# Performance work log

Hardware: AMD Instinct MI355X
Metric: run time of the kernel (lower is better)

The kernel has to match this reference:

```python
import jax, jax.numpy as jnp
import numpy as np
from jax import lax

DN = ('NCHW', 'OIHW', 'NCHW')


def setup_inputs() -> dict:
    key = jax.random.key(0)
    k1, k2 = jax.random.split(key)
    x = jax.random.uniform(k1, (32, 3, 128, 128), dtype=jnp.float32)
    # kaiming-uniform-like filters; the module zeroes the first filter after init
    fan_in = 1 * 7 * 7
    bound = np.sqrt(6.0 / ((1 + 5.0) * fan_in))  # kaiming_uniform with a=sqrt(5)
    weight = jax.random.uniform(k2, (512, 1, 7, 7), minval=-bound, maxval=bound,
                                dtype=jnp.float32)
    weight = weight.at[0].set(0.0)
    std = jnp.asarray(2.0, dtype=jnp.float32)
    return {"x": x, "weight": weight, "std": std}


def _rbf_dist_conv(gray, weight, std, stride=1):
    # ||window - filter||^2 = ||window||^2 + ||filter||^2 - 2 * window . filter
    strides = (stride, stride)
    xw = lax.conv_general_dilated(gray, weight, strides, 'VALID',
                                  dimension_numbers=DN)       # [B,O,OH,OW]
    ones_k = jnp.ones((1, 1) + weight.shape[2:], gray.dtype)
    x2 = lax.conv_general_dilated(gray * gray, ones_k, strides, 'VALID',
                                  dimension_numbers=DN)       # [B,1,OH,OW]
    w2 = jnp.sum(weight * weight, axis=(1, 2, 3))[None, :, None, None]
    sq = jnp.maximum(x2 + w2 - 2.0 * xw, 0.0)
    dist = jnp.sqrt(sq)                                        # torch.cdist
    # gauss RBF: exp(-d^2 / (2*std^2))
    return jnp.exp(-(dist * dist) / (2.0 * std * std))


def reference(x, weight, std):
    # forward converts 3-channel input to grayscale (ITU-R 601 weights, as torchvision)
    gray = (0.2989 * x[:, 0] + 0.587 * x[:, 1] + 0.114 * x[:, 2])[:, None]  # [B,1,H,W]
    return _rbf_dist_conv(gray, weight, std, stride=1)
```

## Files before the change

### kernel.cpp

```cpp
#include <hip/hip_runtime.h>

typedef _Float16 half_t;
typedef __attribute__((ext_vector_type(8))) _Float16 half8;
typedef __attribute__((ext_vector_type(4))) float f32x4;

#define NB 32
#define NH 128
#define NW 128
#define NOH 122
#define NOW 122
#define NOC 512
#define NTAP 49
#define KPAD 64


__global__ __launch_bounds__(256) void k_gray(const float* __restrict__ x,
                                              half_t* __restrict__ gh) {
    int t = blockIdx.x * 256 + threadIdx.x;
    if (t >= NB * NH * NW) return;
    int b = t >> 14;
    int pix = t & 16383;
    const float* xb = x + (size_t)b * 3 * 16384;
    float g = 0.2989f * xb[pix] + 0.587f * xb[16384 + pix] + 0.114f * xb[32768 + pix];
    gh[t] = (half_t)g;
}

__global__ __launch_bounds__(64) void k_w(const float* __restrict__ w,
                                          half_t* __restrict__ Wh,
                                          float* __restrict__ w2) {
    int o = blockIdx.x * 64 + threadIdx.x;
    if (o >= NOC) return;
    float s = 0.f;
    for (int t = 0; t < KPAD; ++t) {
        float v = (t < NTAP) ? w[o * NTAP + t] : 0.f;
        half_t h = (half_t)v;
        Wh[o * KPAD + t] = h;
        float f = (float)h;
        s += f * f;
    }
    w2[o] = s;
}

__global__ __launch_bounds__(256) void k_x2(const half_t* __restrict__ gh,
                                            float* __restrict__ x2) {
    int t = blockIdx.x * 256 + threadIdx.x;
    if (t >= NB * NOH * NOW) return;
    int b = t / (NOH * NOW);
    int rem = t - b * (NOH * NOW);
    int oh = rem / NOW;
    int ow = rem - oh * NOW;
    const half_t* g = gh + ((size_t)b * NH + oh) * NW + ow;
    float s = 0.f;
#pragma unroll
    for (int kh = 0; kh < 7; ++kh) {
#pragma unroll
        for (int kw = 0; kw < 7; ++kw) {
            float v = (float)g[kh * NW + kw];
            s += v * v;
        }
    }
    x2[t] = s;
}

__global__ __launch_bounds__(256) void k_main(const half_t* __restrict__ gh,
                                              const half_t* __restrict__ Wh,
                                              const float* __restrict__ w2,
                                              const float* __restrict__ x2,
                                              const float* __restrict__ stdp,
                                              float* __restrict__ out) {
    const int fg = blockIdx.x;
    const int oh = blockIdx.y;
    const int b  = blockIdx.z;

    __shared__ half_t gS[10][136];

    const int tid = threadIdx.x;
    for (int idx = tid; idx < 10 * 136; idx += 256) {
        int r = idx / 136;
        int c = idx - r * 136;
        half_t hv = (half_t)0.f;
        if (r < 7 && c < 128) hv = gh[((size_t)b * NH + (oh + r)) * NW + c];
        gS[r][c] = hv;
    }

    const int wave = tid >> 6;
    const int lane = tid & 63;
    const int col  = lane & 15;
    const int kq   = lane >> 4;
    const int n0   = wave * 32;

    half8 afrag[4][2];
#pragma unroll
    for (int mi = 0; mi < 4; ++mi) {
#pragma unroll
        for (int ks = 0; ks < 2; ++ks) {
            const half_t* ap = Wh + ((size_t)(fg * 64 + mi * 16 + col) * KPAD + ks * 32 + kq * 8);
            afrag[mi][ks] = *(const half8*)ap;
        }
    }

    __syncthreads();

    half8 bfrag[2][2];
#pragma unroll
    for (int ni = 0; ni < 2; ++ni) {
#pragma unroll
        for (int ks = 0; ks < 2; ++ks) {
            half8 v;
#pragma unroll
            for (int i = 0; i < 8; ++i) {
                int t = ks * 32 + kq * 8 + i;
                int kh = (t * 37) >> 8;
                int kw = t - kh * 7;
                v[i] = gS[kh][n0 + ni * 16 + col + kw];
            }
            bfrag[ni][ks] = v;
        }
    }

    f32x4 acc[4][2];
#pragma unroll
    for (int mi = 0; mi < 4; ++mi)
#pragma unroll
        for (int ni = 0; ni < 2; ++ni) {
            f32x4 z = {0.f, 0.f, 0.f, 0.f};
            acc[mi][ni] = z;
        }

#pragma unroll
    for (int ks = 0; ks < 2; ++ks)
#pragma unroll
        for (int mi = 0; mi < 4; ++mi)
#pragma unroll
            for (int ni = 0; ni < 2; ++ni)
                acc[mi][ni] = __builtin_amdgcn_mfma_f32_16x16x32_f16(
                    afrag[mi][ks], bfrag[ni][ks], acc[mi][ni], 0, 0, 0);

    const float sv = stdp[0];
    const float inv2s2 = 0.5f / (sv * sv);

#pragma unroll
    for (int ni = 0; ni < 2; ++ni) {
        const int p = n0 + ni * 16 + col;
        const bool pok = p < NOW;
        const float x2v = pok ? x2[((size_t)b * NOH + oh) * NOW + p] : 0.f;
#pragma unroll
        for (int mi = 0; mi < 4; ++mi) {
#pragma unroll
            for (int r = 0; r < 4; ++r) {
                const int o = fg * 64 + mi * 16 + kq * 4 + r;
                float sq = x2v + w2[o] - 2.f * acc[mi][ni][r];
                sq = fmaxf(sq, 0.f);
                float res = __expf(-sq * inv2s2);
                if (pok) out[(((size_t)b * NOC + o) * NOH + oh) * NOW + p] = res;
            }
        }
    }
}

extern "C" void kernel_launch(void* const* d_in, const int* in_sizes, int n_in,
                              void* d_out, int out_size, void* d_ws, size_t ws_size,
                              hipStream_t stream) {
    const float* x    = (const float*)d_in[0];
    const float* w    = (const float*)d_in[1];
    const float* stdp = (const float*)d_in[2];
    float* out = (float*)d_out;

    char* ws = (char*)d_ws;
    half_t* gh = (half_t*)ws;
    half_t* Wh = (half_t*)(ws + 1048576);
    float*  w2 = (float*)(ws + 1114112);
    float*  x2 = (float*)(ws + 1116160);

    k_gray<<<(NB * NH * NW + 255) / 256, 256, 0, stream>>>(x, gh);
    k_w<<<(NOC + 63) / 64, 64, 0, stream>>>(w, Wh, w2);
    k_x2<<<(NB * NOH * NOW + 255) / 256, 256, 0, stream>>>(gh, x2);

    dim3 grid(8, NOH, NB);
    k_main<<<grid, 256, 0, stream>>>(gh, Wh, w2, x2, stdp, out);
}
```

Measured before the change: 367.4 us.

## Process multiple output rows per block with rolling LDS row buffer

Each block now handles a chunk of 31 output rows instead of one. It keeps an 8-row ring buffer of the grayscale image in shared memory and loads only one new row per iteration. Filter fragments and per-filter squared norms are loaded once into registers and reused across all rows, removing redundant global and LDS fill work per row. The trade-off is a grid shrunk from about 31k blocks to 1024, which lowers parallelism and the number of stores in flight for what is largely an output-write-bound kernel. It also adds a barrier per row.

New measurement: 408.5 us. 1.11x slower.

```diff
diff --git a/kernel.cpp b/kernel.cpp
--- a/kernel.cpp
+++ b/kernel.cpp
@@ -12,6 +12,8 @@
 #define NOC 512
 #define NTAP 49
 #define KPAD 64
+#define NCH 4
+#define RPC 31
 
 
 __global__ __launch_bounds__(256) void k_gray(const float* __restrict__ x,
@@ -69,20 +71,14 @@
                                               const float* __restrict__ stdp,
                                               float* __restrict__ out) {
     const int fg = blockIdx.x;
-    const int oh = blockIdx.y;
+    const int ch = blockIdx.y;
     const int b  = blockIdx.z;
+    const int oh0 = ch * RPC;
+    const int nrows = (NOH - oh0 < RPC) ? (NOH - oh0) : RPC;
 
-    __shared__ half_t gS[10][136];
+    __shared__ half_t gS[8][136];
 
-    const int tid = threadIdx.x;
-    for (int idx = tid; idx < 10 * 136; idx += 256) {
-        int r = idx / 136;
-        int c = idx - r * 136;
-        half_t hv = (half_t)0.f;
-        if (r < 7 && c < 128) hv = gh[((size_t)b * NH + (oh + r)) * NW + c];
-        gS[r][c] = hv;
-    }
-
+    const int tid  = threadIdx.x;
     const int wave = tid >> 6;
     const int lane = tid & 63;
     const int col  = lane & 15;
@@ -91,68 +87,88 @@
 
     half8 afrag[4][2];
 #pragma unroll
-    for (int mi = 0; mi < 4; ++mi) {
+    for (int mi = 0; mi < 4; ++mi)
 #pragma unroll
         for (int ks = 0; ks < 2; ++ks) {
             const half_t* ap = Wh + ((size_t)(fg * 64 + mi * 16 + col) * KPAD + ks * 32 + kq * 8);
             afrag[mi][ks] = *(const half8*)ap;
         }
-    }
 
-    __syncthreads();
+    f32x4 w2c[4];
+#pragma unroll
+    for (int mi = 0; mi < 4; ++mi)
+        w2c[mi] = *(const f32x4*)(w2 + fg * 64 + mi * 16 + kq * 4);
 
-    half8 bfrag[2][2];
-#pragma unroll
-    for (int ni = 0; ni < 2; ++ni) {
-#pragma unroll
-        for (int ks = 0; ks < 2; ++ks) {
-            half8 v;
-#pragma unroll
-            for (int i = 0; i < 8; ++i) {
-                int t = ks * 32 + kq * 8 + i;
-                int kh = (t * 37) >> 8;
-                int kw = t - kh * 7;
-                v[i] = gS[kh][n0 + ni * 16 + col + kw];
-            }
-            bfrag[ni][ks] = v;
+    for (int idx = tid; idx < 7 * 136; idx += 256) {
+        int r = idx / 136;
+        int c = idx - r * 136;
+        if (r < 6) {
+            half_t hv = (c < 128) ? gh[((size_t)b * NH + (oh0 + r)) * NW + c] : (half_t)0.f;
+            gS[(oh0 + r) & 7][c] = hv;
+        } else {
+            gS[(oh0 + 7) & 7][c] = (half_t)0.f;
         }
     }
-
-    f32x4 acc[4][2];
-#pragma unroll
-    for (int mi = 0; mi < 4; ++mi)
-#pragma unroll
-        for (int ni = 0; ni < 2; ++ni) {
-            f32x4 z = {0.f, 0.f, 0.f, 0.f};
-            acc[mi][ni] = z;
-        }
-
-#pragma unroll
-    for (int ks = 0; ks < 2; ++ks)
-#pragma unroll
-        for (int mi = 0; mi < 4; ++mi)
-#pragma unroll
-            for (int ni = 0; ni < 2; ++ni)
-                acc[mi][ni] = __builtin_amdgcn_mfma_f32_16x16x32_f16(
-                    afrag[mi][ks], bfrag[ni][ks], acc[mi][ni], 0, 0, 0);
 
     const float sv = stdp[0];
     const float inv2s2 = 0.5f / (sv * sv);
 
+    for (int oh = oh0; oh < oh0 + nrows; ++oh) {
+        if (tid < 136) {
+            int row = oh + 6;
+            half_t hv = (tid < 128) ? gh[((size_t)b * NH + row) * NW + tid] : (half_t)0.f;
+            gS[row & 7][tid] = hv;
+        }
+        __syncthreads();
+
+        half8 bfrag[2][2];
 #pragma unroll
-    for (int ni = 0; ni < 2; ++ni) {
-        const int p = n0 + ni * 16 + col;
-        const bool pok = p < NOW;
-        const float x2v = pok ? x2[((size_t)b * NOH + oh) * NOW + p] : 0.f;
+        for (int ni = 0; ni < 2; ++ni)
 #pragma unroll
-        for (int mi = 0; mi < 4; ++mi) {
+            for (int ks = 0; ks < 2; ++ks) {
+                half8 v;
 #pragma unroll
-            for (int r = 0; r < 4; ++r) {
-                const int o = fg * 64 + mi * 16 + kq * 4 + r;
-                float sq = x2v + w2[o] - 2.f * acc[mi][ni][r];
-                sq = fmaxf(sq, 0.f);
-                float res = __expf(-sq * inv2s2);
-                if (pok) out[(((size_t)b * NOC + o) * NOH + oh) * NOW + p] = res;
+                for (int i = 0; i < 8; ++i) {
+                    int t = ks * 32 + kq * 8 + i;
+                    int kh = (t * 37) >> 8;
+                    int kw = t - kh * 7;
+                    v[i] = gS[(oh + kh) & 7][n0 + ni * 16 + col + kw];
+                }
+                bfrag[ni][ks] = v;
+            }
+
+        f32x4 acc[4][2];
+#pragma unroll
+        for (int mi = 0; mi < 4; ++mi)
+#pragma unroll
+            for (int ni = 0; ni < 2; ++ni) {
+                f32x4 z = {0.f, 0.f, 0.f, 0.f};
+                acc[mi][ni] = z;
+            }
+
+#pragma unroll
+        for (int ks = 0; ks < 2; ++ks)
+#pragma unroll
+            for (int mi = 0; mi < 4; ++mi)
+#pragma unroll
+                for (int ni = 0; ni < 2; ++ni)
+                    acc[mi][ni] = __builtin_amdgcn_mfma_f32_16x16x32_f16(
+                        afrag[mi][ks], bfrag[ni][ks], acc[mi][ni], 0, 0, 0);
+
+#pragma unroll
+        for (int ni = 0; ni < 2; ++ni) {
+            const int p = n0 + ni * 16 + col;
+            const bool pok = p < NOW;
+            const float x2v = pok ? x2[((size_t)b * NOH + oh) * NOW + p] : 0.f;
+#pragma unroll
+            for (int mi = 0; mi < 4; ++mi) {
+#pragma unroll
+                for (int r = 0; r < 4; ++r) {
+                    const int o = fg * 64 + mi * 16 + kq * 4 + r;
+                    float sq = fmaxf(fmaf(-2.f, acc[mi][ni][r], x2v + w2c[mi][r]), 0.f);
+                    float res = __expf(-sq * inv2s2);
+                    if (pok) out[(((size_t)b * NOC + o) * NOH + oh) * NOW + p] = res;
+                }
             }
         }
     }
@@ -176,6 +192,6 @@
     k_w<<<(NOC + 63) / 64, 64, 0, stream>>>(w, Wh, w2);
     k_x2<<<(NB * NOH * NOW + 255) / 256, 256, 0, stream>>>(gh, x2);
 
-    dim3 grid(8, NOH, NB);
+    dim3 grid(8, NCH, NB);
     k_main<<<grid, 256, 0, stream>>>(gh, Wh, w2, x2, stdp, out);
 }
```

## Pad filter taps to 8x8 and swap MFMA operands for vectorized output stores

Applied to the files above, without the earlier changes.

Filter taps are re-laid out as 8 rows of 8 so each lane's K-chunk maps to one image row, which makes the shared-memory gather contiguous and needs fewer staged rows. MFMA operands are swapped so each lane holds four consecutive output pixels, letting the output and x2 loads use 16-byte vector accesses instead of scalar ones. The grayscale kernel is vectorized 4-wide, and the window-energy computation is split into separable row and column sums through an extra buffer. This adds one kernel launch and extra workspace traffic, but the main kernel is bound by output writes, which this is meant to speed up.

Result: slower. 407.8 us (+11.0%).

```diff
diff --git a/kernel.cpp b/kernel.cpp
--- a/kernel.cpp
+++ b/kernel.cpp
@@ -1,6 +1,7 @@
 #include <hip/hip_runtime.h>
 
 typedef _Float16 half_t;
+typedef __attribute__((ext_vector_type(4))) _Float16 half4;
 typedef __attribute__((ext_vector_type(8))) _Float16 half8;
 typedef __attribute__((ext_vector_type(4))) float f32x4;
 
@@ -10,19 +11,24 @@
 #define NOH 122
 #define NOW 122
 #define NOC 512
-#define NTAP 49
 #define KPAD 64
 
 
 __global__ __launch_bounds__(256) void k_gray(const float* __restrict__ x,
                                               half_t* __restrict__ gh) {
     int t = blockIdx.x * 256 + threadIdx.x;
-    if (t >= NB * NH * NW) return;
-    int b = t >> 14;
-    int pix = t & 16383;
-    const float* xb = x + (size_t)b * 3 * 16384;
-    float g = 0.2989f * xb[pix] + 0.587f * xb[16384 + pix] + 0.114f * xb[32768 + pix];
-    gh[t] = (half_t)g;
+    if (t >= NB * NH * NW / 4) return;
+    int b = t >> 12;
+    int pix4 = t & 4095;
+    const float* xb = x + (size_t)b * 3 * 16384 + pix4 * 4;
+    f32x4 r = *(const f32x4*)xb;
+    f32x4 g = *(const f32x4*)(xb + 16384);
+    f32x4 bl = *(const f32x4*)(xb + 32768);
+    half4 o;
+#pragma unroll
+    for (int i = 0; i < 4; ++i)
+        o[i] = (half_t)(0.2989f * r[i] + 0.587f * g[i] + 0.114f * bl[i]);
+    *(half4*)(gh + (size_t)t * 4) = o;
 }
 
 __global__ __launch_bounds__(64) void k_w(const float* __restrict__ w,
@@ -32,7 +38,8 @@
     if (o >= NOC) return;
     float s = 0.f;
     for (int t = 0; t < KPAD; ++t) {
-        float v = (t < NTAP) ? w[o * NTAP + t] : 0.f;
+        int kh = t >> 3, kw = t & 7;
+        float v = (kh < 7 && kw < 7) ? w[o * 49 + kh * 7 + kw] : 0.f;
         half_t h = (half_t)v;
         Wh[o * KPAD + t] = h;
         float f = (float)h;
@@ -41,24 +48,36 @@
     w2[o] = s;
 }
 
-__global__ __launch_bounds__(256) void k_x2(const half_t* __restrict__ gh,
+__global__ __launch_bounds__(256) void k_rs(const half_t* __restrict__ gh,
+                                            float* __restrict__ Sg) {
+    int t = blockIdx.x * 256 + threadIdx.x;
+    if (t >= NB * NH * NOW) return;
+    int b = t / (NH * NOW);
+    int rem = t - b * (NH * NOW);
+    int h = rem / NOW;
+    int p = rem - h * NOW;
+    const half_t* g = gh + ((size_t)b * NH + h) * NW + p;
+    float s = 0.f;
+#pragma unroll
+    for (int kw = 0; kw < 7; ++kw) {
+        float v = (float)g[kw];
+        s += v * v;
+    }
+    Sg[t] = s;
+}
+
+__global__ __launch_bounds__(256) void k_x2(const float* __restrict__ Sg,
                                             float* __restrict__ x2) {
     int t = blockIdx.x * 256 + threadIdx.x;
     if (t >= NB * NOH * NOW) return;
     int b = t / (NOH * NOW);
     int rem = t - b * (NOH * NOW);
     int oh = rem / NOW;
-    int ow = rem - oh * NOW;
-    const half_t* g = gh + ((size_t)b * NH + oh) * NW + ow;
+    int p = rem - oh * NOW;
+    const float* s0 = Sg + ((size_t)b * NH + oh) * NOW + p;
     float s = 0.f;
 #pragma unroll
-    for (int kh = 0; kh < 7; ++kh) {
-#pragma unroll
-        for (int kw = 0; kw < 7; ++kw) {
-            float v = (float)g[kh * NW + kw];
-            s += v * v;
-        }
-    }
+    for (int kh = 0; kh < 7; ++kh) s += s0[kh * NOW];
     x2[t] = s;
 }
 
@@ -72,10 +91,10 @@
     const int oh = blockIdx.y;
     const int b  = blockIdx.z;
 
-    __shared__ half_t gS[10][136];
+    __shared__ half_t gS[8][136];
 
     const int tid = threadIdx.x;
-    for (int idx = tid; idx < 10 * 136; idx += 256) {
+    for (int idx = tid; idx < 8 * 136; idx += 256) {
         int r = idx / 136;
         int c = idx - r * 136;
         half_t hv = (half_t)0.f;
@@ -89,40 +108,35 @@
     const int kq   = lane >> 4;
     const int n0   = wave * 32;
 
-    half8 afrag[4][2];
-#pragma unroll
-    for (int mi = 0; mi < 4; ++mi) {
+    half8 wfrag[4][2];
+#pragma unroll
+    for (int ni = 0; ni < 4; ++ni)
+#pragma unroll
+        for (int ks = 0; ks < 2; ++ks)
+            wfrag[ni][ks] = *(const half8*)(Wh + ((size_t)(fg * 64 + ni * 16 + col) * KPAD
+                                                  + (ks * 4 + kq) * 8));
+
+    __syncthreads();
+
+    half8 afrag[2][2];
+#pragma unroll
+    for (int mi = 0; mi < 2; ++mi) {
+        const int p = n0 + mi * 16 + col;
 #pragma unroll
         for (int ks = 0; ks < 2; ++ks) {
-            const half_t* ap = Wh + ((size_t)(fg * 64 + mi * 16 + col) * KPAD + ks * 32 + kq * 8);
-            afrag[mi][ks] = *(const half8*)ap;
+            const half_t* src = &gS[ks * 4 + kq][p];
+            half8 v;
+#pragma unroll
+            for (int i = 0; i < 8; ++i) v[i] = src[i];
+            afrag[mi][ks] = v;
         }
     }
 
-    __syncthreads();
-
-    half8 bfrag[2][2];
-#pragma unroll
-    for (int ni = 0; ni < 2; ++ni) {
-#pragma unroll
-        for (int ks = 0; ks < 2; ++ks) {
-            half8 v;
-#pragma unroll
-            for (int i = 0; i < 8; ++i) {
-                int t = ks * 32 + kq * 8 + i;
-                int kh = (t * 37) >> 8;
-                int kw = t - kh * 7;
-                v[i] = gS[kh][n0 + ni * 16 + col + kw];
-            }
-            bfrag[ni][ks] = v;
-        }
-    }
-
-    f32x4 acc[4][2];
-#pragma unroll
-    for (int mi = 0; mi < 4; ++mi)
-#pragma unroll
-        for (int ni = 0; ni < 2; ++ni) {
+    f32x4 acc[2][4];
+#pragma unroll
+    for (int mi = 0; mi < 2; ++mi)
+#pragma unroll
+        for (int ni = 0; ni < 4; ++ni) {
             f32x4 z = {0.f, 0.f, 0.f, 0.f};
             acc[mi][ni] = z;
         }
@@ -130,29 +144,38 @@
 #pragma unroll
     for (int ks = 0; ks < 2; ++ks)
 #pragma unroll
-        for (int mi = 0; mi < 4; ++mi)
-#pragma unroll
-            for (int ni = 0; ni < 2; ++ni)
+        for (int mi = 0; mi < 2; ++mi)
+#pragma unroll
+            for (int ni = 0; ni < 4; ++ni)
                 acc[mi][ni] = __builtin_amdgcn_mfma_f32_16x16x32_f16(
-                    afrag[mi][ks], bfrag[ni][ks], acc[mi][ni], 0, 0, 0);
+                    afrag[mi][ks], wfrag[ni][ks], acc[mi][ni], 0, 0, 0);
 
     const float sv = stdp[0];
     const float inv2s2 = 0.5f / (sv * sv);
-
-#pragma unroll
-    for (int ni = 0; ni < 2; ++ni) {
-        const int p = n0 + ni * 16 + col;
-        const bool pok = p < NOW;
-        const float x2v = pok ? x2[((size_t)b * NOH + oh) * NOW + p] : 0.f;
-#pragma unroll
-        for (int mi = 0; mi < 4; ++mi) {
+    const size_t rowBase = ((size_t)b * NOH + oh) * NOW;
+
+#pragma unroll
+    for (int mi = 0; mi < 2; ++mi) {
+        const int p0 = n0 + mi * 16 + kq * 4;
+        if (p0 >= NOW) continue;
+        const f32x4 x2v = *(const f32x4*)(x2 + rowBase + p0);
+#pragma unroll
+        for (int ni = 0; ni < 4; ++ni) {
+            const int o = fg * 64 + ni * 16 + col;
+            const float w2v = w2[o];
+            f32x4 res;
 #pragma unroll
             for (int r = 0; r < 4; ++r) {
-                const int o = fg * 64 + mi * 16 + kq * 4 + r;
-                float sq = x2v + w2[o] - 2.f * acc[mi][ni][r];
-                sq = fmaxf(sq, 0.f);
-                float res = __expf(-sq * inv2s2);
-                if (pok) out[(((size_t)b * NOC + o) * NOH + oh) * NOW + p] = res;
+                float sq = fmaxf(fmaf(-2.f, acc[mi][ni][r], x2v[r] + w2v), 0.f);
+                res[r] = __expf(-sq * inv2s2);
+            }
+            float* dst = out + (((size_t)b * NOC + o) * NOH + oh) * NOW + p0;
+            if (p0 + 3 < NOW) {
+                *(f32x4*)dst = res;
+            } else {
+#pragma unroll
+                for (int r = 0; r < 4; ++r)
+                    if (p0 + r < NOW) dst[r] = res[r];
             }
         }
     }
@@ -171,10 +194,12 @@
     half_t* Wh = (half_t*)(ws + 1048576);
     float*  w2 = (float*)(ws + 1114112);
     float*  x2 = (float*)(ws + 1116160);
-
-    k_gray<<<(NB * NH * NW + 255) / 256, 256, 0, stream>>>(x, gh);
+    float*  Sg = (float*)(ws + 3021440);
+
+    k_gray<<<(NB * NH * NW / 4 + 255) / 256, 256, 0, stream>>>(x, gh);
     k_w<<<(NOC + 63) / 64, 64, 0, stream>>>(w, Wh, w2);
-    k_x2<<<(NB * NOH * NOW + 255) / 256, 256, 0, stream>>>(gh, x2);
+    k_rs<<<(NB * NH * NOW + 255) / 256, 256, 0, stream>>>(gh, Sg);
+    k_x2<<<(NB * NOH * NOW + 255) / 256, 256, 0, stream>>>(Sg, x2);
 
     dim3 grid(8, NOH, NB);
     k_main<<<grid, 256, 0, stream>>>(gh, Wh, w2, x2, stdp, out);
```
